# Kernel tuning notes

Measured on AMD Instinct MI355X. Metric: run time of the kernel, lower is better.

Reference implementation:

```python
import jax, jax.numpy as jnp
import numpy as np

B, S, D_IN, D_OUT = 4, 2048, 1024, 1024
N_TREES, DEPTH, N_HEADS = 12, 3, 3
N_INTERNAL = 2 ** DEPTH - 1  # 7
N_LEAVES = 2 ** DEPTH        # 8
TEMPERATURE = 1.0
SOFTPLUS_SHIFT = 0.5413      # softplus(0.5413) ~= 1.0, so init node temp ~ 1


def _build_path_indices(depth):
    """Root-to-leaf internal-node indices and go-left directions per leaf."""
    L = 2 ** depth
    pi = np.zeros((L, depth), np.int32)
    pd = np.zeros((L, depth), np.float32)
    for leaf in range(L):
        node = 0
        for d in range(depth):
            pi[leaf, d] = node
            bit = (leaf >> (depth - 1 - d)) & 1
            pd[leaf, d] = 1.0 - bit
            node = 2 * node + 1 + bit
    return pi, pd


def setup_inputs() -> dict:
    key = jax.random.key(0)
    ks = jax.random.split(key, 4)
    x = jax.random.normal(ks[0], (B, S, D_IN), dtype=jnp.float32)
    # normal(0, 0.1) routing init
    decision_weights = 0.1 * jax.random.normal(ks[1], (N_TREES, N_INTERNAL, D_IN), dtype=jnp.float32)
    decision_biases = jnp.zeros((N_TREES, N_INTERNAL), dtype=jnp.float32)
    node_temperature_logits = jnp.zeros((N_TREES, N_INTERNAL), dtype=jnp.float32)
    # nn.Linear default init ~ U(-1/sqrt(D), 1/sqrt(D)); use matching-scale normal
    gate_w = jax.random.normal(ks[2], (N_TREES, D_IN), dtype=jnp.float32) / np.sqrt(D_IN)
    gate_b = jnp.zeros((N_TREES,), dtype=jnp.float32)
    # xavier_normal over each [n_leaves, output_dim] slice
    xav_std = np.sqrt(2.0 / (N_LEAVES + D_OUT))
    leaf_outputs = xav_std * jax.random.normal(ks[3], (N_HEADS, N_TREES, N_LEAVES, D_OUT), dtype=jnp.float32)
    pi, pd = _build_path_indices(DEPTH)
    return {
        "x": x,
        "decision_weights": decision_weights,
        "decision_biases": decision_biases,
        "node_temperature_logits": node_temperature_logits,
        "gate_w": gate_w,
        "gate_b": gate_b,
        "leaf_outputs": leaf_outputs,
        "path_indices": jnp.asarray(pi),
        "path_dirs": jnp.asarray(pd),
    }


def reference(x, decision_weights, decision_biases, node_temperature_logits,
              gate_w, gate_b, leaf_outputs, path_indices, path_dirs):
    # decisions: [B, S, T, N_internal]
    decisions = jnp.einsum('bsd,tnd->bstn', x, decision_weights) + decision_biases
    node_temps = TEMPERATURE * jax.nn.softplus(node_temperature_logits + SOFTPLUS_SHIFT)
    decisions = jax.nn.sigmoid(decisions / node_temps)
    # gather nodes along each root->leaf path: [B, S, T, L, depth]
    relevant = decisions[..., path_indices]
    probs_per_level = path_dirs * relevant + (1.0 - path_dirs) * (1.0 - relevant)
    leaf_probs = probs_per_level.prod(axis=-1)  # [B, S, T, L]
    # softmax gate over trees: [B, S, T]
    weights = jax.nn.softmax(jnp.einsum('bsd,td->bst', x, gate_w) + gate_b, axis=-1)
    # fold tree gate into leaf probs, then contract leaves against leaf outputs
    routed = leaf_probs * weights[..., None]            # [B, S, T, L]
    out = jnp.einsum('bstl,htld->hbsd', routed, leaf_outputs)  # [H, B, S, Dout]
    return out
```

## Files before the change

### kernel.cpp

```cpp
#include <hip/hip_runtime.h>

typedef __attribute__((ext_vector_type(8))) short short8;
typedef __attribute__((ext_vector_type(4))) float floatx4;
typedef unsigned int uint;
typedef unsigned short ushort;
typedef __attribute__((ext_vector_type(4))) uint uintx4;

#define NTOK   8192
#define DIN    1024
#define DOUT   1024
#define NJ     96
#define TOKPB  16
#define DSTR   97
#define SSTR   85
#define RSTR   104
#define LOT_H  (DOUT * NJ)

static __device__ inline ushort f2b(float f) {
    uint u = __builtin_bit_cast(uint, f);
    u = u + 0x7fffu + ((u >> 16) & 1u);
    return (ushort)(u >> 16);
}
static __device__ inline uint pack2(float a, float b) {
    return (uint)f2b(a) | ((uint)f2b(b) << 16);
}

__global__ __launch_bounds__(256) void k_prep(const float* __restrict__ lo,
                                              const float* __restrict__ dw,
                                              const float* __restrict__ gw,
                                              ushort* __restrict__ lot,
                                              ushort* __restrict__ wcat) {
    int i = blockIdx.x * 256 + threadIdx.x;
    if (i < 3 * LOT_H) {
        int h = i / LOT_H;
        int rem = i - h * LOT_H;
        int k = rem >> 10;
        int d = rem & 1023;
        lot[h * LOT_H + d * NJ + k] = f2b(lo[i]);
    } else {
        int j = i - 3 * LOT_H;
        int r = j >> 10, c = j & 1023;
        float v = (r < 84) ? dw[r * DIN + c] : gw[(r - 84) * DIN + c];
        wcat[j] = f2b(v);
    }
}

__global__ __launch_bounds__(256, 2) void k_fused(
    const float* __restrict__ x,
    const ushort* __restrict__ wcat,
    const float* __restrict__ db,
    const float* __restrict__ ntl,
    const float* __restrict__ gb,
    const int*   __restrict__ pi,
    const float* __restrict__ pd,
    const ushort* __restrict__ lot,
    float* __restrict__ out)
{
    __shared__ float decis[TOKPB * DSTR];
    __shared__ float sdecs[TOKPB * SSTR];
    __shared__ __attribute__((aligned(16))) ushort rt[TOKPB][RSTR];
    __shared__ float invt[84];
    __shared__ float biasf[96];
    __shared__ int   pis[24];
    __shared__ float pds[24];

    const int tid = threadIdx.x;
    const int tb  = blockIdx.x * TOKPB;

    if (tid < 84) {
        float z = ntl[tid] + 0.5413f;
        float sp = (z > 20.0f) ? z : log1pf(__expf(z));
        invt[tid]  = 1.0f / sp;
        biasf[tid] = db[tid];
    } else if (tid < 96) {
        biasf[tid] = gb[tid - 84];
    } else if (tid < 120) {
        pis[tid - 96] = pi[tid - 96];
    } else if (tid < 144) {
        pds[tid - 120] = pd[tid - 120];
    }

    const int wave = tid >> 6, lane = tid & 63;
    const int lrow = lane & 15, quad = lane >> 4;

    const int nt0 = wave;
    const bool two = (wave < 2);
    const int nt1 = wave + 4;

    floatx4 acc0 = (floatx4)(0.0f), acc1 = (floatx4)(0.0f);

    const float*  xr = x    + (size_t)(tb + lrow) * DIN + quad * 8;
    const ushort* w0 = wcat + (size_t)(nt0 * 16 + lrow) * DIN + quad * 8;
    const ushort* w1 = wcat + (size_t)(nt1 * 16 + lrow) * DIN + quad * 8;

#pragma unroll
    for (int kc = 0; kc < 8; ++kc) {
        short8 a[4];
#pragma unroll
        for (int kt = 0; kt < 4; ++kt) {
            floatx4 u = *(const floatx4*)(xr + kc * 128 + kt * 32);
            floatx4 v = *(const floatx4*)(xr + kc * 128 + kt * 32 + 4);
            union { short8 s; uint w[4]; } pk;
            pk.w[0] = pack2(u[0], u[1]);
            pk.w[1] = pack2(u[2], u[3]);
            pk.w[2] = pack2(v[0], v[1]);
            pk.w[3] = pack2(v[2], v[3]);
            a[kt] = pk.s;
        }
#pragma unroll
        for (int kt = 0; kt < 4; ++kt) {
            short8 b0 = *(const short8*)(w0 + kc * 128 + kt * 32);
            acc0 = __builtin_amdgcn_mfma_f32_16x16x32_bf16(a[kt], b0, acc0, 0, 0, 0);
        }
        if (two) {
#pragma unroll
            for (int kt = 0; kt < 4; ++kt) {
                short8 b1 = *(const short8*)(w1 + kc * 128 + kt * 32);
                acc1 = __builtin_amdgcn_mfma_f32_16x16x32_bf16(a[kt], b1, acc1, 0, 0, 0);
            }
        }
    }

#pragma unroll
    for (int r = 0; r < 4; ++r)
        decis[(quad * 4 + r) * DSTR + nt0 * 16 + lrow] = acc0[r];
    if (two) {
#pragma unroll
        for (int r = 0; r < 4; ++r)
            decis[(quad * 4 + r) * DSTR + nt1 * 16 + lrow] = acc1[r];
    }
    __syncthreads();

#pragma unroll
    for (int i = 0; i < 6; ++i) {
        int idx = tid + 256 * i;
        if (idx < TOKPB * 84) {
            int tk = idx / 84, nd = idx - tk * 84;
            float dv = (decis[tk * DSTR + nd] + biasf[nd]) * invt[nd];
            sdecs[tk * SSTR + nd] = 1.0f / (1.0f + __expf(-dv));
        }
    }
    __syncthreads();

    {
        const int tk = tid >> 4, l = (tid >> 1) & 7, th = tid & 1;
        float g[12], gm = -1e30f;
#pragma unroll
        for (int tt = 0; tt < 12; ++tt) {
            g[tt] = decis[tk * DSTR + 84 + tt] + biasf[84 + tt];
            gm = fmaxf(gm, g[tt]);
        }
        float gs = 0.0f;
#pragma unroll
        for (int tt = 0; tt < 12; ++tt) { g[tt] = __expf(g[tt] - gm); gs += g[tt]; }
        float ginv = 1.0f / gs;

        const int   n0 = pis[l * 3 + 0], n1 = pis[l * 3 + 1], n2 = pis[l * 3 + 2];
        const float d0 = pds[l * 3 + 0], d1 = pds[l * 3 + 1], d2 = pds[l * 3 + 2];
        const float* sd = sdecs + tk * SSTR;
        const int t0 = th * 6;
#pragma unroll
        for (int t = 0; t < 6; ++t) {
            int tt = t0 + t;
            float s0 = sd[tt * 7 + n0], s1 = sd[tt * 7 + n1], s2 = sd[tt * 7 + n2];
            float pb = g[tt] * ginv
                     * (d0 * s0 + (1.0f - d0) * (1.0f - s0))
                     * (d1 * s1 + (1.0f - d1) * (1.0f - s1))
                     * (d2 * s2 + (1.0f - d2) * (1.0f - s2));
            rt[tk][tt * 8 + l] = f2b(pb);
        }
    }
    __syncthreads();

    {
        short8 a[3];
#pragma unroll
        for (int kk = 0; kk < 3; ++kk)
            a[kk] = *(const short8*)(&rt[lrow][quad * 8 + kk * 32]);

        short8 bb[3][6];
#define LOADB(B, G) do { \
    _Pragma("unroll") for (int q_ = 0; q_ < 2; ++q_) { \
        int c_ = wave * 768 + ((G) * 2 + q_) * 16; \
        int h_ = c_ >> 10; \
        int d_ = (c_ & 1023) + lrow; \
        const ushort* bp_ = lot + (size_t)h_ * LOT_H + (size_t)d_ * NJ + quad * 8; \
        _Pragma("unroll") for (int kk_ = 0; kk_ < 3; ++kk_) \
            bb[B][q_ * 3 + kk_] = *(const short8*)(bp_ + kk_ * 32); \
    } } while (0)

        LOADB(0, 0);
        LOADB(1, 1);
#pragma unroll
        for (int g = 0; g < 24; ++g) {
            const int cur = g % 3;
            if (g < 22) LOADB((g + 2) % 3, g + 2);
#pragma unroll
            for (int q = 0; q < 2; ++q) {
                floatx4 c0 = (floatx4)(0.0f);
#pragma unroll
                for (int kk = 0; kk < 3; ++kk)
                    c0 = __builtin_amdgcn_mfma_f32_16x16x32_bf16(a[kk], bb[cur][q * 3 + kk], c0, 0, 0, 0);
                int c = wave * 768 + (g * 2 + q) * 16;
                int h = c >> 10;
                int d = (c & 1023) + lrow;
                float* ob = out + ((size_t)h * NTOK + tb) * DOUT + d;
#pragma unroll
                for (int r = 0; r < 4; ++r)
                    __builtin_nontemporal_store(c0[r], ob + (size_t)(quad * 4 + r) * DOUT);
            }
        }
#undef LOADB
    }
}

extern "C" void kernel_launch(void* const* d_in, const int* in_sizes, int n_in,
                              void* d_out, int out_size, void* d_ws, size_t ws_size,
                              hipStream_t stream) {
    const float* x   = (const float*)d_in[0];
    const float* dw  = (const float*)d_in[1];
    const float* db  = (const float*)d_in[2];
    const float* ntl = (const float*)d_in[3];
    const float* gw  = (const float*)d_in[4];
    const float* gb  = (const float*)d_in[5];
    const float* lo  = (const float*)d_in[6];
    const int*   pi  = (const int*)d_in[7];
    const float* pd  = (const float*)d_in[8];
    float* out = (float*)d_out;

    ushort* lot  = (ushort*)d_ws;
    ushort* wcat = lot + (size_t)3 * LOT_H;

    k_prep<<<dim3((3 * LOT_H + NJ * DIN) / 256), dim3(256), 0, stream>>>(lo, dw, gw, lot, wcat);
    k_fused<<<dim3(NTOK / TOKPB), dim3(256), 0, stream>>>(x, wcat, db, ntl, gb, pi, pd, lot, out);
}
```

Before: 173.5 us.

## Tile leaf-output layout and swap MFMA operands for vectorized output stores

Leaf outputs are stored in 16x32 tiles so each wave reads contiguous 512-element blocks for the B operand. The MFMA operands are swapped so each lane holds four consecutive output columns of one token row, which allows a single 16-byte store instead of four scalar nontemporal stores. Prefetch depth drops from two groups to one tile ahead. The trade-off is less latency hiding on loads and the loss of the nontemporal store hint.

```diff
diff --git a/kernel.cpp b/kernel.cpp
--- a/kernel.cpp
+++ b/kernel.cpp
@@ -36,7 +36,8 @@
         int rem = i - h * LOT_H;
         int k = rem >> 10;
         int d = rem & 1023;
-        lot[h * LOT_H + d * NJ + k] = f2b(lo[i]);
+        int off = (((d >> 4) * 3 + (k >> 5)) << 9) + ((d & 15) << 5) + (k & 31);
+        lot[h * LOT_H + off] = f2b(lo[i]);
     } else {
         int j = i - 3 * LOT_H;
         int r = j >> 10, c = j & 1023;
@@ -173,44 +174,39 @@
     __syncthreads();
 
     {
-        short8 a[3];
+        short8 ar[3];
 #pragma unroll
         for (int kk = 0; kk < 3; ++kk)
-            a[kk] = *(const short8*)(&rt[lrow][quad * 8 + kk * 32]);
-
-        short8 bb[3][6];
-#define LOADB(B, G) do { \
-    _Pragma("unroll") for (int q_ = 0; q_ < 2; ++q_) { \
-        int c_ = wave * 768 + ((G) * 2 + q_) * 16; \
+            ar[kk] = *(const short8*)(&rt[lrow][quad * 8 + kk * 32]);
+
+        const int tilebase = wave * 768;
+        short8 bl[2][3];
+#define LOADT(B, T) do { \
+        int c_ = tilebase + (T) * 16; \
         int h_ = c_ >> 10; \
-        int d_ = (c_ & 1023) + lrow; \
-        const ushort* bp_ = lot + (size_t)h_ * LOT_H + (size_t)d_ * NJ + quad * 8; \
-        _Pragma("unroll") for (int kk_ = 0; kk_ < 3; ++kk_) \
-            bb[B][q_ * 3 + kk_] = *(const short8*)(bp_ + kk_ * 32); \
-    } } while (0)
-
-        LOADB(0, 0);
-        LOADB(1, 1);
-#pragma unroll
-        for (int g = 0; g < 24; ++g) {
-            const int cur = g % 3;
-            if (g < 22) LOADB((g + 2) % 3, g + 2);
-#pragma unroll
-            for (int q = 0; q < 2; ++q) {
-                floatx4 c0 = (floatx4)(0.0f);
-#pragma unroll
-                for (int kk = 0; kk < 3; ++kk)
-                    c0 = __builtin_amdgcn_mfma_f32_16x16x32_bf16(a[kk], bb[cur][q * 3 + kk], c0, 0, 0, 0);
-                int c = wave * 768 + (g * 2 + q) * 16;
-                int h = c >> 10;
-                int d = (c & 1023) + lrow;
-                float* ob = out + ((size_t)h * NTOK + tb) * DOUT + d;
-#pragma unroll
-                for (int r = 0; r < 4; ++r)
-                    __builtin_nontemporal_store(c0[r], ob + (size_t)(quad * 4 + r) * DOUT);
-            }
-        }
-#undef LOADB
+        int dt_ = (c_ & 1023) >> 4; \
+        const ushort* p_ = lot + (size_t)h_ * LOT_H + ((size_t)(dt_ * 3) << 9) \
+                         + (lrow << 5) + quad * 8; \
+        bl[B][0] = *(const short8*)(p_); \
+        bl[B][1] = *(const short8*)(p_ + 512); \
+        bl[B][2] = *(const short8*)(p_ + 1024); \
+    } while (0)
+
+        LOADT(0, 0);
+#pragma unroll
+        for (int t = 0; t < 48; ++t) {
+            const int cur = t & 1;
+            if (t < 47) LOADT(cur ^ 1, t + 1);
+            floatx4 c = (floatx4)(0.0f);
+#pragma unroll
+            for (int kk = 0; kk < 3; ++kk)
+                c = __builtin_amdgcn_mfma_f32_16x16x32_bf16(bl[cur][kk], ar[kk], c, 0, 0, 0);
+            const int col = tilebase + t * 16;
+            const int h = col >> 10;
+            const int d = (col & 1023) + quad * 4;
+            *(floatx4*)(out + ((size_t)h * NTOK + tb + lrow) * DOUT + d) = c;
+        }
+#undef LOADT
     }
 }
 
```

New measurement: 170.8 us. About the same (-1.5%).
